# Kernel tuning notes

Measured on AMD Instinct MI355X. Metric: run time of the kernel, lower is better.

## Reference

```python
import jax, jax.numpy as jnp
import numpy as np
from jax import lax

N_SECTIONS, N_CHANNELS = 8, 128
KT, KF = 32, 16                 # kernel (time, freq)
LPOST = 400                     # section_length_postsyn
LPRE = KT + LPOST - 1           # 431, section_length_presyn
SECTION_DISTANCE = 400          # LPRE - overlap (overlap = 31)
N_TIMESTEPS, FREQ = 3231, 256
THRESHOLD = 15.0


def setup_inputs() -> dict:
    key = jax.random.key(0)
    k1, k2 = jax.random.split(key)
    # scale so mean conv response ~ threshold (512 taps * 0.8 * mean(X))
    X = jax.random.uniform(k1, (N_TIMESTEPS, FREQ), dtype=jnp.float32) * 0.073
    # SpykeTorch Convolution init: N(0.8, 0.05)
    W = 0.8 + 0.05 * jax.random.normal(k2, (N_SECTIONS, N_CHANNELS, 1, KT, KF), dtype=jnp.float32)
    return {"X": X, "W": W}


def _sections(X):
    # [S, LPRE, FREQ] overlapping time windows
    starts = jnp.arange(N_SECTIONS) * SECTION_DISTANCE
    idx = starts[:, None] + jnp.arange(LPRE)
    return X[idx]


def _conv_sections(X, W):
    Xs = _sections(X)  # [S, LPRE, FREQ]
    def conv1(xs, w):
        # xs: [LPRE, FREQ], w: [C, 1, KT, KF] -> [C, LPOST, FOUT]
        return lax.conv_general_dilated(xs[None, None], w, (1, 1), 'VALID')[0]
    return jax.vmap(conv1)(Xs, W)  # [S, C, LPOST, FOUT]


def reference(X, W):
    pots = _conv_sections(X, W)                              # [S, C, 400, 241]
    # sf.fire: zero potentials < threshold, then sign -> binary spikes
    spikes = (pots >= THRESHOLD).astype(pots.dtype)
    # Pooling((LPOST, KF)): max-pool, stride = window, no padding
    pool = lax.reduce_window(spikes, -jnp.inf, lax.max,
                             (1, 1, LPOST, KF), (1, 1, LPOST, KF), 'VALID')  # [S, C, 1, 15]
    # sf.get_k_winners(pool): dim 0 (sections) acts as the time dimension
    T = pool.shape[0]
    spk = jnp.sign(pool)
    earliest = jnp.clip((T - spk.sum(axis=0)).astype(jnp.int32), 0, T - 1)   # [C,1,Fp]
    values = jnp.take_along_axis(pool, earliest[None], axis=0)[0]            # earliest spike value
    trunc = spk * values[None]
    v = trunc.max() * T
    trunc = trunc + spk * v
    total = trunc.sum(axis=0)                                # [C, 1, Fp]
    max_val = total.max()
    # winners[0][0] = feature (channel) index of the flat argmax
    feat = jnp.argmax(total.reshape(-1)) // (total.shape[1] * total.shape[2])
    return jnp.where(max_val != 0, feat, -1).astype(jnp.int32)
```

## Files before the change

### kernel.cpp

```cpp
#include <hip/hip_runtime.h>


using int2v  = __attribute__((ext_vector_type(2))) int;
using int4v  = __attribute__((ext_vector_type(4))) int;
using int8v  = __attribute__((ext_vector_type(8))) int;
using f32x8  = __attribute__((ext_vector_type(8))) float;
using f32x16 = __attribute__((ext_vector_type(16))) float;

#define SCALE_ONE 0x7F7F7F7F
#define THRESH_Q  4920.0f

#if __has_builtin(__builtin_amdgcn_cvt_scalef32_pk_fp4_f32)
#define HWFP4 1
#else
#define HWFP4 0
#endif

__device__ __forceinline__ unsigned f4enc(float v) {
  float r2 = __builtin_rintf(v + v);
  float r1 = __builtin_rintf(v);
  return (v <= 2.f) ? (unsigned)r2
       : (v <= 4.f) ? (unsigned)r1 + 2u
       : (v < 5.f)  ? 6u : 7u;
}

__device__ __forceinline__ unsigned pack8(f32x8 v) {
  unsigned d = 0;
#if HWFP4
  d = __builtin_amdgcn_cvt_scalef32_pk_fp4_f32(d, v[0], v[1], 1.0f, 0);
  d = __builtin_amdgcn_cvt_scalef32_pk_fp4_f32(d, v[2], v[3], 1.0f, 1);
  d = __builtin_amdgcn_cvt_scalef32_pk_fp4_f32(d, v[4], v[5], 1.0f, 2);
  d = __builtin_amdgcn_cvt_scalef32_pk_fp4_f32(d, v[6], v[7], 1.0f, 3);
#else
#pragma unroll
  for (int e = 0; e < 8; ++e) d |= f4enc(v[e]) << (4 * e);
#endif
  return d;
}

__global__ __launch_bounds__(256) void prep_kernel(const float* __restrict__ W,
                                                   unsigned char* __restrict__ Wp4,
                                                   unsigned* __restrict__ pool) {
  int t = blockIdx.x * 256 + threadIdx.x;
  if (t < 1024) pool[t] = 0;
  int s = t >> 11, r = t & 2047, c = r >> 4, b = r & 15;
  const float* src = W + ((s * 128 + c) * 512 + b * 32);
  int4v o;
#pragma unroll
  for (int i = 0; i < 4; ++i) {
    f32x8 sv;
#pragma unroll
    for (int e = 0; e < 8; ++e) sv[e] = fmaxf(src[i * 8 + e], 0.f) * 4.f;
    o[i] = (int)pack8(sv);
  }
  *(int4v*)(Wp4 + s * 32768 + (b >> 1) * 4096 + (b & 1) * 2048 + c * 16) = o;
}

__global__ __launch_bounds__(512, 2) void conv_pool_kernel(const float* __restrict__ X,
                                                           const unsigned char* __restrict__ Wp4,
                                                           unsigned* __restrict__ pool) {
  __shared__ __align__(16) unsigned char Ash[2][8 * 512];
  __shared__ unsigned poolmask[128];

  const int tid = threadIdx.x;
  const int s   = blockIdx.x & 7;
  const int lb  = blockIdx.x >> 3;
  const int NT  = (lb < 6) ? 13 : 12;

  const int w = tid >> 6, l = tid & 63;
  const int m31 = l & 31, ko = l >> 5;

  if (tid < 128) poolmask[tid] = 0;
  __syncthreads();

  const int rA  = l >> 1, hA = l & 1;
  const int okB = l < 62;
  const int rB  = okB ? 32 + (l >> 1) : 62;
  const int col = w + hA * 8;
  const int sA  = w * 512 + rA * 8 + hA * 4;
  const int sB  = w * 512 + (32 + (l >> 1)) * 8 + hA * 4;
  const float* Xrow = X + (s * 400) * 256 + col;

  const int aoff = w * 512 + m31 * 8 + ko * 16;

  f32x8 xa, xb;
  {
    int tau = lb, tt = tau / 30, ft = tau % 30;
    int t0 = (tt == 12) ? 368 : tt * 32;
    const float* pa = Xrow + (t0 + rA) * 256 + ft * 8;
    const float* pb = Xrow + (t0 + rB) * 256 + ft * 8;
#pragma unroll
    for (int e = 0; e < 8; ++e) { xa[e] = pa[e]; xb[e] = pb[e]; }
  }
  __builtin_amdgcn_sched_barrier(0);

  int4v Breg[8][4];
  {
    const unsigned char* wb = Wp4 + s * 32768 + ko * 2048 + m31 * 16;
#pragma unroll
    for (int ch = 0; ch < 8; ++ch)
#pragma unroll
      for (int nt = 0; nt < 4; ++nt)
        Breg[ch][nt] = *(const int4v*)(wb + ch * 4096 + nt * 512);
  }

  *(unsigned*)&Ash[0][sA] = pack8(xa * 82.f);
  if (okB) *(unsigned*)&Ash[0][sB] = pack8(xb * 82.f);
  if (NT > 1) {
    int tau = lb + 32, tt = tau / 30, ft = tau % 30;
    int t0 = (tt == 12) ? 368 : tt * 32;
    const float* pa = Xrow + (t0 + rA) * 256 + ft * 8;
    const float* pb = Xrow + (t0 + rB) * 256 + ft * 8;
#pragma unroll
    for (int e = 0; e < 8; ++e) { xa[e] = pa[e]; xb[e] = pb[e]; }
  }

  unsigned pm[4] = {0, 0, 0, 0};

#pragma unroll 1
  for (int i = 0; i < NT; ++i) {
    const unsigned char* rb = &Ash[i & 1][0];
    unsigned char* wbuf = &Ash[(i + 1) & 1][0];

    if (i + 1 < NT) {
      *(unsigned*)&wbuf[sA] = pack8(xa * 82.f);
      if (okB) *(unsigned*)&wbuf[sB] = pack8(xb * 82.f);
    }
    if (i + 2 < NT) {
      int tau = lb + 32 * (i + 2), tt = tau / 30, ft = tau % 30;
      int t0 = (tt == 12) ? 368 : tt * 32;
      const float* pa = Xrow + (t0 + rA) * 256 + ft * 8;
      const float* pb = Xrow + (t0 + rB) * 256 + ft * 8;
#pragma unroll
      for (int e = 0; e < 8; ++e) { xa[e] = pa[e]; xb[e] = pb[e]; }
    }

    f32x16 acc[4];
#pragma unroll
    for (int b = 0; b < 4; ++b)
#pragma unroll
      for (int e = 0; e < 16; ++e) acc[b][e] = 0.f;
#pragma unroll
    for (int ch = 0; ch < 8; ++ch) {
      int2v alo = *(const int2v*)&rb[aoff + ch * 32];
      int2v ahi = *(const int2v*)&rb[aoff + ch * 32 + 8];
      int8v Af = {alo[0], alo[1], ahi[0], ahi[1], 0, 0, 0, 0};
#pragma unroll
      for (int nt = 0; nt < 4; ++nt) {
        int8v Bf = {Breg[ch][nt][0], Breg[ch][nt][1],
                    Breg[ch][nt][2], Breg[ch][nt][3], 0, 0, 0, 0};
        acc[nt] = __builtin_amdgcn_mfma_scale_f32_32x32x64_f8f6f4(
            Af, Bf, acc[nt], 4, 4, 0, SCALE_ONE, 0, SCALE_ONE);
      }
    }

    unsigned sp = 0;
#pragma unroll
    for (int nt = 0; nt < 4; ++nt) {
      float m0 = -1e30f;
#pragma unroll
      for (int e = 0; e < 16; ++e) m0 = fmaxf(m0, acc[nt][e]);
      if (m0 >= THRESH_Q) sp |= (1u << nt);
    }
    sp |= __shfl_xor(sp, 32, 64);
    {
      int fp = ((lb + 32 * i) % 30) >> 1;
#pragma unroll
      for (int nt = 0; nt < 4; ++nt)
        pm[nt] |= ((sp >> nt) & 1u) << fp;
    }
  }

  if (l < 32) {
#pragma unroll
    for (int nt = 0; nt < 4; ++nt)
      if (pm[nt]) atomicOr(&poolmask[nt * 32 + m31], pm[nt]);
  }
  __syncthreads();
  if (tid < 128) {
    unsigned m = poolmask[tid];
    if (m) atomicOr(&pool[s * 128 + tid], m);
  }
}

__global__ __launch_bounds__(256) void winner_kernel(const unsigned* __restrict__ pool,
                                                     float* __restrict__ out) {
  __shared__ unsigned pb[1024];
  __shared__ int bestpk;
  int tid = threadIdx.x;
  if (tid == 0) bestpk = 0;
  for (int q = tid; q < 1024; q += 256) pb[q] = pool[q];
  __syncthreads();

  int lbest = 0;
  for (int p = tid; p < 1920; p += 256) {
    int c = p / 15, f = p % 15;
    int cnt = 0;
#pragma unroll
    for (int s2 = 0; s2 < 8; ++s2) cnt += (pb[s2 * 128 + c] >> f) & 1;
    if (cnt > 0) {
      int early = 8 - cnt;
      int val = (pb[early * 128 + c] >> f) & 1;
      int total = cnt * (8 + val);
      int pack = (total << 12) | (4095 - p);
      if (pack > lbest) lbest = pack;
    }
  }
  atomicMax(&bestpk, lbest);
  __syncthreads();
  if (tid == 0) {
    int feat = (4095 - (bestpk & 4095)) / 15;
    out[0] = (bestpk != 0) ? (float)feat : -1.0f;
  }
}

extern "C" void kernel_launch(void* const* d_in, const int* in_sizes, int n_in,
                              void* d_out, int out_size, void* d_ws, size_t ws_size,
                              hipStream_t stream) {
  (void)in_sizes; (void)n_in; (void)out_size; (void)ws_size;
  const float* X = (const float*)d_in[0];
  const float* W = (const float*)d_in[1];
  unsigned char* Wp4 = (unsigned char*)d_ws;
  unsigned* pool = (unsigned*)((char*)d_ws + (1 << 18));

  prep_kernel<<<64, 256, 0, stream>>>(W, Wp4, pool);
  conv_pool_kernel<<<256, 512, 0, stream>>>(X, Wp4, pool);
  winner_kernel<<<1, 256, 0, stream>>>(pool, (float*)d_out);
}
```

Before: 83.83 us.

## Stage X tiles through LDS with coalesced vector loads and deeper prefetch

Each wave used to gather its own strided X elements with scalar loads. Now the whole block loads the 64x32 X tile with coalesced float4 loads into a padded LDS buffer. Each thread then reads its column from LDS and packs it to FP4. The prefetch distance grows to three tiles, using register double-buffering and a loop unrolled by two. This cuts uncoalesced global traffic, at the cost of extra LDS space and a block-wide barrier every tile.

After: 85.37 us. About the same (+1.8%).

```diff
diff --git a/kernel.cpp b/kernel.cpp
--- a/kernel.cpp
+++ b/kernel.cpp
@@ -4,6 +4,7 @@
 using int2v  = __attribute__((ext_vector_type(2))) int;
 using int4v  = __attribute__((ext_vector_type(4))) int;
 using int8v  = __attribute__((ext_vector_type(8))) int;
+using f32x4  = __attribute__((ext_vector_type(4))) float;
 using f32x8  = __attribute__((ext_vector_type(8))) float;
 using f32x16 = __attribute__((ext_vector_type(16))) float;
 
@@ -60,6 +61,7 @@
                                                            const unsigned char* __restrict__ Wp4,
                                                            unsigned* __restrict__ pool) {
   __shared__ __align__(16) unsigned char Ash[2][8 * 512];
+  __shared__ float Xsh[2][64 * 33];
   __shared__ unsigned poolmask[128];
 
   const int tid = threadIdx.x;
@@ -70,28 +72,42 @@
   const int w = tid >> 6, l = tid & 63;
   const int m31 = l & 31, ko = l >> 5;
 
-  if (tid < 128) poolmask[tid] = 0;
-  __syncthreads();
+  const int cr = tid >> 3;
+  const int cc = (tid & 7) * 4;
 
   const int rA  = l >> 1, hA = l & 1;
   const int okB = l < 62;
   const int rB  = okB ? 32 + (l >> 1) : 62;
-  const int col = w + hA * 8;
+  const int xcol = w + hA * 8;
   const int sA  = w * 512 + rA * 8 + hA * 4;
-  const int sB  = w * 512 + (32 + (l >> 1)) * 8 + hA * 4;
-  const float* Xrow = X + (s * 400) * 256 + col;
-
+  const int sB  = w * 512 + rB * 8 + hA * 4;
   const int aoff = w * 512 + m31 * 8 + ko * 16;
 
-  f32x8 xa, xb;
-  {
-    int tau = lb, tt = tau / 30, ft = tau % 30;
+  if (tid < 128) poolmask[tid] = 0;
+
+  auto issue_load = [&](int i, f32x4& cv) {
+    int tau = lb + 32 * i, tt = tau / 30, ft = tau % 30;
     int t0 = (tt == 12) ? 368 : tt * 32;
-    const float* pa = Xrow + (t0 + rA) * 256 + ft * 8;
-    const float* pb = Xrow + (t0 + rB) * 256 + ft * 8;
-#pragma unroll
-    for (int e = 0; e < 8; ++e) { xa[e] = pa[e]; xb[e] = pb[e]; }
-  }
+    int row = s * 400 + t0 + cr; if (row > 3230) row = 3230;
+    int cb = ft * 8 + cc; if (cb > 252) cb = 252;
+    cv = *(const f32x4*)(X + row * 256 + cb);
+  };
+  auto store_x = [&](int buf, f32x4& cv) {
+#pragma unroll
+    for (int j = 0; j < 4; ++j) Xsh[buf][cr * 33 + cc + j] = cv[j];
+  };
+  auto convert = [&](int buf) {
+    const float* xs = &Xsh[buf][0];
+    f32x8 va, vb;
+    int ia = rA * 33 + xcol, ib = rB * 33 + xcol;
+#pragma unroll
+    for (int e = 0; e < 8; ++e) { va[e] = xs[ia + e] * 82.f; vb[e] = xs[ib + e] * 82.f; }
+    *(unsigned*)&Ash[buf][sA] = pack8(va);
+    if (okB) *(unsigned*)&Ash[buf][sB] = pack8(vb);
+  };
+
+  f32x4 cvA, cvB;
+  issue_load(0, cvA);
   __builtin_amdgcn_sched_barrier(0);
 
   int4v Breg[8][4];
@@ -104,36 +120,17 @@
         Breg[ch][nt] = *(const int4v*)(wb + ch * 4096 + nt * 512);
   }
 
-  *(unsigned*)&Ash[0][sA] = pack8(xa * 82.f);
-  if (okB) *(unsigned*)&Ash[0][sB] = pack8(xb * 82.f);
-  if (NT > 1) {
-    int tau = lb + 32, tt = tau / 30, ft = tau % 30;
-    int t0 = (tt == 12) ? 368 : tt * 32;
-    const float* pa = Xrow + (t0 + rA) * 256 + ft * 8;
-    const float* pb = Xrow + (t0 + rB) * 256 + ft * 8;
-#pragma unroll
-    for (int e = 0; e < 8; ++e) { xa[e] = pa[e]; xb[e] = pb[e]; }
-  }
+  store_x(0, cvA);
+  if (NT > 1) issue_load(1, cvA);
+  __syncthreads();
+  convert(0);
+  if (NT > 1) { store_x(1, cvA); if (NT > 2) issue_load(2, cvA); }
+  __syncthreads();
 
   unsigned pm[4] = {0, 0, 0, 0};
 
-#pragma unroll 1
-  for (int i = 0; i < NT; ++i) {
-    const unsigned char* rb = &Ash[i & 1][0];
-    unsigned char* wbuf = &Ash[(i + 1) & 1][0];
-
-    if (i + 1 < NT) {
-      *(unsigned*)&wbuf[sA] = pack8(xa * 82.f);
-      if (okB) *(unsigned*)&wbuf[sB] = pack8(xb * 82.f);
-    }
-    if (i + 2 < NT) {
-      int tau = lb + 32 * (i + 2), tt = tau / 30, ft = tau % 30;
-      int t0 = (tt == 12) ? 368 : tt * 32;
-      const float* pa = Xrow + (t0 + rA) * 256 + ft * 8;
-      const float* pb = Xrow + (t0 + rB) * 256 + ft * 8;
-#pragma unroll
-      for (int e = 0; e < 8; ++e) { xa[e] = pa[e]; xb[e] = pb[e]; }
-    }
+  auto tile_body = [&](int i, int par, f32x4& cvS, f32x4& cvI) {
+    if (i + 3 < NT) issue_load(i + 3, cvI);
 
     f32x16 acc[4];
 #pragma unroll
@@ -142,8 +139,8 @@
       for (int e = 0; e < 16; ++e) acc[b][e] = 0.f;
 #pragma unroll
     for (int ch = 0; ch < 8; ++ch) {
-      int2v alo = *(const int2v*)&rb[aoff + ch * 32];
-      int2v ahi = *(const int2v*)&rb[aoff + ch * 32 + 8];
+      int2v alo = *(const int2v*)&Ash[par][aoff + ch * 32];
+      int2v ahi = *(const int2v*)&Ash[par][aoff + ch * 32 + 8];
       int8v Af = {alo[0], alo[1], ahi[0], ahi[1], 0, 0, 0, 0};
 #pragma unroll
       for (int nt = 0; nt < 4; ++nt) {
@@ -169,6 +166,16 @@
       for (int nt = 0; nt < 4; ++nt)
         pm[nt] |= ((sp >> nt) & 1u) << fp;
     }
+
+    if (i + 1 < NT) convert(par ^ 1);
+    if (i + 2 < NT) store_x(par, cvS);
+    if (i + 1 < NT) __syncthreads();
+  };
+
+#pragma unroll 1
+  for (int i = 0; i < NT; i += 2) {
+    tile_body(i, 0, cvA, cvB);
+    if (i + 1 < NT) tile_body(i + 1, 1, cvB, cvA);
   }
 
   if (l < 32) {
```
